# Kernel tuning notes

Hardware: AMD Instinct MI355X
Metric: run time of the kernel (lower is better)

The kernel has to match this reference:

```python
import jax, jax.numpy as jnp
import numpy as np

DIM, QS, NH, WS, SS, FFW = 256, 56, 8, 7, 3, 1024


def _make_attn_mask(H, W, ws, ss):
    # Swin-style shifted-window attention mask, [nWin, ws*ws, ws*ws]
    img = np.zeros((H, W))
    cnt = 0
    for hs in (slice(0, -ws), slice(-ws, -ss), slice(-ss, None)):
        for wsl in (slice(0, -ws), slice(-ws, -ss), slice(-ss, None)):
            img[hs, wsl] = cnt
            cnt += 1
    mw = img.reshape(H // ws, ws, W // ws, ws).transpose(0, 2, 1, 3).reshape(-1, ws * ws)
    am = mw[:, None, :] - mw[:, :, None]
    return jnp.asarray(np.where(am != 0, -100.0, 0.0), jnp.float32)

ATTN_MASK = _make_attn_mask(QS, QS, WS, SS)


def setup_inputs() -> dict:
    key = jax.random.key(0)
    ks = jax.random.split(key, 16)
    s = lambda fan: 1.0 / np.sqrt(fan)
    return {
        'x': jax.random.normal(ks[0], (16, DIM, QS, QS), jnp.float32),
        'ln1_g': jnp.ones((DIM,), jnp.float32),
        'ln1_b': jnp.zeros((DIM,), jnp.float32),
        'ln2_g': jnp.ones((DIM,), jnp.float32),
        'ln2_b': jnp.zeros((DIM,), jnp.float32),
        'qkv_w': jax.random.normal(ks[1], (DIM, 3 * DIM), jnp.float32) * s(DIM),
        'qkv_b': jnp.zeros((3 * DIM,), jnp.float32),
        'proj_w': jax.random.normal(ks[2], (DIM, DIM), jnp.float32) * s(DIM),
        'proj_b': jnp.zeros((DIM,), jnp.float32),
        'ffn_w1': jax.random.normal(ks[3], (DIM, FFW), jnp.float32) * s(DIM),
        'ffn_b1': jnp.zeros((FFW,), jnp.float32),
        'ffn_w2': jax.random.normal(ks[4], (FFW, DIM), jnp.float32) * s(FFW),
        'ffn_b2': jnp.zeros((DIM,), jnp.float32),
        'layer_scale': jax.random.normal(ks[5], (DIM,), jnp.float32),
    }


def _ln(t, g, b):
    m = t.mean(-1, keepdims=True)
    v = ((t - m) ** 2).mean(-1, keepdims=True)
    return (t - m) * jax.lax.rsqrt(v + 1e-5) * g + b


def reference(x, ln1_g, ln1_b, ln2_g, ln2_b, qkv_w, qkv_b, proj_w, proj_b,
              ffn_w1, ffn_b1, ffn_w2, ffn_b2, layer_scale):
    B, C, H, W = x.shape
    nh, ws, ss = NH, WS, SS
    hd = C // nh
    nHw, nWw = H // ws, W // ws
    xh = jnp.transpose(x, (0, 2, 3, 1))  # B H W C

    # --- shifted window attention ---
    h = _ln(xh, ln1_g, ln1_b)
    h = jnp.roll(h, (-ss, -ss), axis=(1, 2))
    # window partition: [B, nWin, L, C]
    h = h.reshape(B, nHw, ws, nWw, ws, C).transpose(0, 1, 3, 2, 4, 5)
    h = h.reshape(B, nHw * nWw, ws * ws, C)
    qkv = h @ qkv_w + qkv_b
    q, k, v = jnp.split(qkv, 3, axis=-1)
    L = ws * ws
    q = q.reshape(B, -1, L, nh, hd).transpose(0, 1, 3, 2, 4)  # B W h L d
    k = k.reshape(B, -1, L, nh, hd).transpose(0, 1, 3, 2, 4)
    v = v.reshape(B, -1, L, nh, hd).transpose(0, 1, 3, 2, 4)
    attn = jnp.einsum('bwhid,bwhjd->bwhij', q, k) * (hd ** -0.5)
    attn = attn + ATTN_MASK[None, :, None]  # mask per window index
    attn = jax.nn.softmax(attn, axis=-1)
    o = jnp.einsum('bwhij,bwhjd->bwhid', attn, v)
    o = o.transpose(0, 1, 3, 2, 4).reshape(B, nHw * nWw, L, C)
    o = o @ proj_w + proj_b
    # reverse partition + roll back
    o = o.reshape(B, nHw, nWw, ws, ws, C).transpose(0, 1, 3, 2, 4, 5).reshape(B, H, W, C)
    o = jnp.roll(o, (ss, ss), axis=(1, 2))
    x1 = xh + o

    # --- FFN ---
    h2 = _ln(x1, ln2_g, ln2_b)
    f = jax.nn.relu(h2 @ ffn_w1 + ffn_b1) @ ffn_w2 + ffn_b2
    f = f * layer_scale
    out = x1 + f
    return jnp.transpose(out, (0, 3, 1, 2))  # back to B C H W
```

## Files before the change

### kernel.cpp

```cpp
#include <hip/hip_runtime.h>
#include <hip/hip_bf16.h>
#include <math.h>

typedef unsigned short u16;
typedef __bf16 bf16x8 __attribute__((ext_vector_type(8)));
typedef float  f32x4  __attribute__((ext_vector_type(4)));

#define DIMC 256
#define QSZ  56
#define WSZ  7
#define SSZ  3
#define LWIN 49
#define NWIN 64
#define HW   3136
#define NTOK 50176
#define FFWD 1024
#define FCH  25088

__device__ __forceinline__ u16 f2bu(float f) {
    __hip_bfloat16 h = __float2bfloat16(f);
    return __builtin_bit_cast(u16, h);
}
__device__ __forceinline__ float bu2f(u16 u) {
    unsigned v = (unsigned)u << 16;
    return __builtin_bit_cast(float, v);
}
__device__ __forceinline__ void gload_lds16(const void* g, void* l) {
    __builtin_amdgcn_global_load_lds((const __attribute__((address_space(1))) void*)g,
                                     (__attribute__((address_space(3))) void*)l, 16, 0, 0);
}

__device__ __forceinline__ int region_of(int h) {
    return (h < 49) ? 0 : ((h < 53) ? 1 : 2);
}

__device__ __forceinline__ int row2tok(int m) {
    int b  = m / (NWIN * LWIN);
    int r  = m - b * (NWIN * LWIN);
    int wi = r / LWIN;
    int p  = r - wi * LWIN;
    int wh = wi >> 3, ww = wi & 7;
    int ph = p / 7,   pw = p - ph * 7;
    int hr = wh * 7 + ph, wr = ww * 7 + pw;
    int hs = hr + SSZ; if (hs >= QSZ) hs -= QSZ;
    int ws2 = wr + SSZ; if (ws2 >= QSZ) ws2 -= QSZ;
    return b * HW + hs * QSZ + ws2;
}

__global__ __launch_bounds__(256) void k_wconv(const float* __restrict__ W,
        u16* __restrict__ Wt, int K, int N) {
    __shared__ float tile[32][33];
    int k0 = blockIdx.x * 32, n0 = blockIdx.y * 32;
    int tx = threadIdx.x & 31, ty = threadIdx.x >> 5;
    for (int kk = ty; kk < 32; kk += 8)
        tile[kk][tx] = W[(size_t)(k0 + kk) * N + n0 + tx];
    __syncthreads();
    for (int nn = ty; nn < 32; nn += 8)
        Wt[(size_t)(n0 + nn) * K + k0 + tx] = f2bu(tile[tx][nn]);
}

__global__ __launch_bounds__(256) void k_ln1(const float* __restrict__ x,
        const float* __restrict__ g, const float* __restrict__ be,
        u16* __restrict__ hln) {
    __shared__ float tile[32][257];
    __shared__ float msh[32], rsh[32];
    int blk = blockIdx.x;
    int b   = blk / 98;
    int hw0 = (blk - b * 98) * 32;
    int t   = threadIdx.x;
    int tx  = t & 31, ty = t >> 5;
    for (int c = ty; c < 256; c += 8)
        tile[tx][c] = x[(size_t)(b * 256 + c) * HW + hw0 + tx];
    __syncthreads();
    int row = t >> 3, sub = t & 7;
    float s = 0.f, sq = 0.f;
    for (int c = sub * 32; c < sub * 32 + 32; ++c) {
        float v = tile[row][c]; s += v; sq += v * v;
    }
    for (int o = 4; o; o >>= 1) { s += __shfl_down(s, o, 8); sq += __shfl_down(sq, o, 8); }
    if (sub == 0) {
        float m   = s * (1.f / 256.f);
        float var = sq * (1.f / 256.f) - m * m;
        msh[row] = m; rsh[row] = rsqrtf(var + 1e-5f);
    }
    __syncthreads();
    float gg = g[t], bb = be[t];
    for (int r2 = 0; r2 < 32; ++r2) {
        float v = tile[r2][t];
        hln[(size_t)(b * HW + hw0 + r2) * 256 + t] = f2bu((v - msh[r2]) * rsh[r2] * gg + bb);
    }
}

__global__ __launch_bounds__(256) void k_ln2t(const float* __restrict__ x,
        u16* __restrict__ x1b, const float* __restrict__ g,
        const float* __restrict__ be, u16* __restrict__ h2) {
    __shared__ float tile[32][257];
    __shared__ float msh[32], rsh[32];
    int blk = blockIdx.x;
    int b   = blk / 98;
    int hw0 = (blk - b * 98) * 32;
    int t   = threadIdx.x;
    int tx  = t & 31, ty = t >> 5;
    for (int c = ty; c < 256; c += 8)
        tile[tx][c] = x[(size_t)(b * 256 + c) * HW + hw0 + tx];
    __syncthreads();
    size_t base = (size_t)b * HW + hw0;
    for (int r2 = 0; r2 < 32; ++r2) {
        float v = tile[r2][t] + bu2f(x1b[(base + r2) * 256 + t]);
        tile[r2][t] = v;
        x1b[(base + r2) * 256 + t] = f2bu(v);
    }
    __syncthreads();
    int row = t >> 3, sub = t & 7;
    float s = 0.f, sq = 0.f;
    for (int c = sub * 32; c < sub * 32 + 32; ++c) {
        float v = tile[row][c]; s += v; sq += v * v;
    }
    for (int o = 4; o; o >>= 1) { s += __shfl_down(s, o, 8); sq += __shfl_down(sq, o, 8); }
    if (sub == 0) {
        float m   = s * (1.f / 256.f);
        float var = sq * (1.f / 256.f) - m * m;
        msh[row] = m; rsh[row] = rsqrtf(var + 1e-5f);
    }
    __syncthreads();
    float gg = g[t], bb = be[t];
    for (int r2 = 0; r2 < 32; ++r2) {
        float v = tile[r2][t];
        h2[(base + r2) * 256 + t] = f2bu((v - msh[r2]) * rsh[r2] * gg + bb);
    }
}

template<int MODE>
__global__ __launch_bounds__(256) void k_mgemm(
        const u16* __restrict__ A, const u16* __restrict__ Bt,
        const float* __restrict__ bias, void* __restrict__ Cv,
        int K, int N, const void* __restrict__ extra,
        const float* __restrict__ extra2, int grow0) {
    __shared__ __align__(16) u16 As[2][128 * 32];
    __shared__ __align__(16) u16 Bs[2][128 * 32];
    const int m0 = blockIdx.x * 128, n0 = blockIdx.y * 128;
    const int t = threadIdx.x, lane = t & 63;
    const int wv = t >> 6, wr = wv >> 1, wc = wv & 1;

    int ar0 = m0 + (t >> 2), ar1 = ar0 + 64;
    if (MODE == 0) { ar0 = row2tok(ar0); ar1 = row2tok(ar1); }
    const u16* gA0 = A  + (size_t)ar0 * K + (t & 3) * 8;
    const u16* gA1 = A  + (size_t)ar1 * K + (t & 3) * 8;
    const u16* gB0 = Bt + (size_t)(n0 + (t >> 2)) * K + (t & 3) * 8;
    const u16* gB1 = Bt + (size_t)(n0 + 64 + (t >> 2)) * K + (t & 3) * 8;

    f32x4 acc[4][4] = {};
    const int ra = wr * 64 + (lane & 15);
    const int rb = wc * 64 + (lane & 15);
    const int ko = (lane >> 4) * 8;
    const int nIter = K >> 5;

    gload_lds16(gA0, As[0] + t * 8);
    gload_lds16(gA1, As[0] + 2048 + t * 8);
    gload_lds16(gB0, Bs[0] + t * 8);
    gload_lds16(gB1, Bs[0] + 2048 + t * 8);

    for (int it = 0; it < nIter; ++it) {
        const int cur = it & 1;
        if (it + 1 < nIter) {
            const int k1 = (it + 1) << 5;
            gload_lds16(gA0 + k1, As[cur ^ 1] + t * 8);
            gload_lds16(gA1 + k1, As[cur ^ 1] + 2048 + t * 8);
            gload_lds16(gB0 + k1, Bs[cur ^ 1] + t * 8);
            gload_lds16(gB1 + k1, Bs[cur ^ 1] + 2048 + t * 8);
            asm volatile("s_waitcnt vmcnt(4)" ::: "memory");
        } else {
            asm volatile("s_waitcnt vmcnt(0)" ::: "memory");
        }
        __builtin_amdgcn_s_barrier();
        __builtin_amdgcn_sched_barrier(0);
        bf16x8 af[4], bfr[4];
#pragma unroll
        for (int i = 0; i < 4; ++i)
            af[i] = *(const bf16x8*)(As[cur] + (ra + i * 16) * 32 + ko);
#pragma unroll
        for (int j = 0; j < 4; ++j)
            bfr[j] = *(const bf16x8*)(Bs[cur] + (rb + j * 16) * 32 + ko);
        asm volatile("s_waitcnt lgkmcnt(0)" ::: "memory");
        __builtin_amdgcn_sched_barrier(0);
        __builtin_amdgcn_s_barrier();
#pragma unroll
        for (int i = 0; i < 4; ++i)
#pragma unroll
            for (int j = 0; j < 4; ++j)
                acc[i][j] = __builtin_amdgcn_mfma_f32_16x16x32_bf16(af[i], bfr[j], acc[i][j], 0, 0, 0);
    }

    const int colb = n0 + wc * 64 + (lane & 15);
    const int rowb = m0 + wr * 64 + ((lane >> 4) * 4);

    if constexpr (MODE == 0) {
        u16* Cb = (u16*)Cv;
#pragma unroll
        for (int j = 0; j < 4; ++j) {
            int col = colb + j * 16; float bj = bias[col];
#pragma unroll
            for (int i = 0; i < 4; ++i) {
                int rw = rowb + i * 16;
#pragma unroll
                for (int r = 0; r < 4; ++r)
                    Cb[(size_t)(rw + r) * N + col] = f2bu(acc[i][j][r] + bj);
            }
        }
    } else if constexpr (MODE == 1) {
        u16* Cb = (u16*)Cv;
        int tok[4][4];
#pragma unroll
        for (int i = 0; i < 4; ++i)
#pragma unroll
            for (int r = 0; r < 4; ++r)
                tok[i][r] = row2tok(rowb + i * 16 + r);
#pragma unroll
        for (int j = 0; j < 4; ++j) {
            int col = colb + j * 16; float bj = bias[col];
#pragma unroll
            for (int i = 0; i < 4; ++i)
#pragma unroll
                for (int r = 0; r < 4; ++r)
                    Cb[(size_t)tok[i][r] * 256 + col] = f2bu(acc[i][j][r] + bj);
        }
    } else if constexpr (MODE == 2) {
        u16* Cb = (u16*)Cv;
#pragma unroll
        for (int j = 0; j < 4; ++j) {
            int col = colb + j * 16; float bj = bias[col];
#pragma unroll
            for (int i = 0; i < 4; ++i) {
                int rw = rowb + i * 16;
#pragma unroll
                for (int r = 0; r < 4; ++r)
                    Cb[(size_t)(rw + r) * N + col] = f2bu(fmaxf(acc[i][j][r] + bj, 0.f));
            }
        }
    } else {
        float* C = (float*)Cv;
        const u16* xr = (const u16*)extra;
#pragma unroll
        for (int j = 0; j < 4; ++j) {
            int col = colb + j * 16;
            float bj = bias[col], lj = extra2[col];
#pragma unroll
            for (int i = 0; i < 4; ++i) {
                int g  = grow0 + rowb + i * 16;
                int b  = g / HW, hw = g - b * HW;
                f32x4 o;
#pragma unroll
                for (int r = 0; r < 4; ++r)
                    o[r] = bu2f(xr[(size_t)(g + r) * 256 + col]) + lj * (acc[i][j][r] + bj);
                *(f32x4*)(C + ((size_t)(b * 256 + col)) * HW + hw) = o;
            }
        }
    }
}

__global__ __launch_bounds__(256, 4) void k_attn(const u16* __restrict__ qkv,
        u16* __restrict__ oattn) {
    __shared__ __align__(16) u16 Pl[4][64 * 72];
    const int wv = threadIdx.x >> 6, lane = threadIdx.x & 63;
    const int task = blockIdx.x * 4 + wv;
    const int head = task & 7, win = task >> 3, wi = win & 63;
    const int rowbase = win * LWIN;
    const int g = lane >> 4, c = lane & 15, ko = g * 8;
    const u16* qb = qkv + (size_t)rowbase * 768 + head * 32;

    bf16x8 qf[4], kf[4];
#pragma unroll
    for (int i = 0; i < 4; ++i) {
        int r0 = i * 16 + c; if (r0 > 48) r0 = 48;
        qf[i] = *(const bf16x8*)(qb + (size_t)r0 * 768 + ko);
        kf[i] = *(const bf16x8*)(qb + (size_t)r0 * 768 + 256 + ko);
    }
    f32x4 s[4][4] = {};
#pragma unroll
    for (int i = 0; i < 4; ++i)
#pragma unroll
        for (int j = 0; j < 4; ++j)
            s[i][j] = __builtin_amdgcn_mfma_f32_16x16x32_bf16(qf[i], kf[j], s[i][j], 0, 0, 0);

    bf16x8 vb[2][2];
#pragma unroll
    for (int j2 = 0; j2 < 2; ++j2) {
        int d = j2 * 16 + c;
#pragma unroll
        for (int h = 0; h < 2; ++h)
#pragma unroll
            for (int tt = 0; tt < 8; ++tt) {
                int k = h * 32 + ko + tt;
                u16 val = (k < LWIN) ? qb[(size_t)k * 768 + 512 + d] : (u16)0;
                vb[j2][h][tt] = __builtin_bit_cast(__bf16, val);
            }
    }

    const int wh7 = (wi >> 3) * 7, ww7 = (wi & 7) * 7;
    int idj[4]; bool jok[4];
#pragma unroll
    for (int j = 0; j < 4; ++j) {
        int col = j * 16 + c;
        jok[j] = col < LWIN;
        int p = jok[j] ? col : 48;
        idj[j] = region_of(wh7 + p / 7) * 3 + region_of(ww7 + p % 7);
    }
#pragma unroll
    for (int i = 0; i < 4; ++i) {
#pragma unroll
        for (int r = 0; r < 4; ++r) {
            int row = i * 16 + g * 4 + r;
            int p = row < LWIN ? row : 48;
            int idi = region_of(wh7 + p / 7) * 3 + region_of(ww7 + p % 7);
            float mx = -1e30f;
#pragma unroll
            for (int j = 0; j < 4; ++j) {
                float tv = jok[j] ? fmaf(s[i][j][r], 0.17677669529663687f,
                                         (idi == idj[j]) ? 0.f : -100.f)
                                  : -1e30f;
                s[i][j][r] = tv;
                mx = fmaxf(mx, tv);
            }
            for (int o = 8; o; o >>= 1) mx = fmaxf(mx, __shfl_xor(mx, o));
            float ps = 0.f;
#pragma unroll
            for (int j = 0; j < 4; ++j) {
                float e = __expf(s[i][j][r] - mx);
                s[i][j][r] = e; ps += e;
            }
            for (int o = 8; o; o >>= 1) ps += __shfl_xor(ps, o);
            float inv = 1.f / ps;
#pragma unroll
            for (int j = 0; j < 4; ++j)
                Pl[wv][row * 72 + j * 16 + c] = f2bu(s[i][j][r] * inv);
        }
    }

    f32x4 o[4][2] = {};
#pragma unroll
    for (int i = 0; i < 4; ++i) {
        bf16x8 pa0 = *(const bf16x8*)(&Pl[wv][(i * 16 + c) * 72 + ko]);
        bf16x8 pa1 = *(const bf16x8*)(&Pl[wv][(i * 16 + c) * 72 + ko + 32]);
#pragma unroll
        for (int j2 = 0; j2 < 2; ++j2) {
            o[i][j2] = __builtin_amdgcn_mfma_f32_16x16x32_bf16(pa0, vb[j2][0], o[i][j2], 0, 0, 0);
            o[i][j2] = __builtin_amdgcn_mfma_f32_16x16x32_bf16(pa1, vb[j2][1], o[i][j2], 0, 0, 0);
        }
    }
#pragma unroll
    for (int i = 0; i < 4; ++i)
#pragma unroll
        for (int r = 0; r < 4; ++r) {
            int row = i * 16 + g * 4 + r;
            if (row < LWIN) {
#pragma unroll
                for (int j2 = 0; j2 < 2; ++j2)
                    oattn[(size_t)(rowbase + row) * 256 + head * 32 + j2 * 16 + c]
                        = f2bu(o[i][j2][r]);
            }
        }
}

extern "C" void kernel_launch(void* const* d_in, const int* in_sizes, int n_in,
                              void* d_out, int out_size, void* d_ws, size_t ws_size,
                              hipStream_t stream) {
    const float* x      = (const float*)d_in[0];
    const float* ln1_g  = (const float*)d_in[1];
    const float* ln1_b  = (const float*)d_in[2];
    const float* ln2_g  = (const float*)d_in[3];
    const float* ln2_b  = (const float*)d_in[4];
    const float* qkv_w  = (const float*)d_in[5];
    const float* qkv_b  = (const float*)d_in[6];
    const float* proj_w = (const float*)d_in[7];
    const float* proj_b = (const float*)d_in[8];
    const float* ffn_w1 = (const float*)d_in[9];
    const float* ffn_b1 = (const float*)d_in[10];
    const float* ffn_w2 = (const float*)d_in[11];
    const float* ffn_b2 = (const float*)d_in[12];
    const float* lscale = (const float*)d_in[13];

    char* wsb = (char*)d_ws;
    u16* wqt  = (u16*)(wsb);
    u16* wpt  = (u16*)(wsb + 393216);
    u16* w1t  = (u16*)(wsb + 524288);
    u16* w2t  = (u16*)(wsb + 1048576);
    u16* P    = (u16*)(wsb + 1572864);
    char* Qb  = wsb + 27262976;
    u16* qkvb = (u16*)Qb;
    u16* x1b  = (u16*)Qb;
    u16* f1c  = (u16*)(Qb + 25690112);

    k_wconv<<<dim3(8, 24), 256, 0, stream>>>(qkv_w, wqt, 256, 768);
    k_wconv<<<dim3(8, 8),  256, 0, stream>>>(proj_w, wpt, 256, 256);
    k_wconv<<<dim3(8, 32), 256, 0, stream>>>(ffn_w1, w1t, 256, 1024);
    k_wconv<<<dim3(32, 8), 256, 0, stream>>>(ffn_w2, w2t, 1024, 256);

    k_ln1<<<16 * 98, 256, 0, stream>>>(x, ln1_g, ln1_b, P);
    k_mgemm<0><<<dim3(392, 6), 256, 0, stream>>>(P, wqt, qkv_b, qkvb, 256, 768,
                                                 nullptr, nullptr, 0);
    k_attn<<<2048, 256, 0, stream>>>(qkvb, P);
    k_mgemm<1><<<dim3(392, 2), 256, 0, stream>>>(P, wpt, proj_b, x1b, 256, 256,
                                                 nullptr, nullptr, 0);
    k_ln2t<<<16 * 98, 256, 0, stream>>>(x, x1b, ln2_g, ln2_b, P);
    for (int c = 0; c < 2; ++c) {
        k_mgemm<2><<<dim3(196, 8), 256, 0, stream>>>(P + (size_t)c * FCH * 256, w1t, ffn_b1,
                                                     f1c, 256, 1024, nullptr, nullptr, 0);
        k_mgemm<3><<<dim3(196, 2), 256, 0, stream>>>(f1c, w2t, ffn_b2, d_out, 1024, 256,
                                                     x1b, lscale, c * FCH);
    }
}
```

Baseline: 279.9 us.

## Enlarge GEMM tile to 256x128 with 512 threads and XOR-swizzle LDS

The bf16 MFMA GEMM now uses blocks of 8 waves that compute a 256x128 output tile. Each B tile is therefore reused across twice as many A rows, and each thread issues fewer global loads per k-step. The order of the 16-byte k-chunks in shared memory is XOR-swizzled by row, and the fragment reads use the matching swizzle, to reduce LDS bank conflicts. The trade-off is half as many blocks per launch and more LDS per block, which may lower occupancy and hurt load balance on the smaller GEMMs.

```diff
diff --git a/kernel.cpp b/kernel.cpp
--- a/kernel.cpp
+++ b/kernel.cpp
@@ -131,44 +131,42 @@
 }
 
 template<int MODE>
-__global__ __launch_bounds__(256) void k_mgemm(
+__global__ __launch_bounds__(512) void k_mgemm(
         const u16* __restrict__ A, const u16* __restrict__ Bt,
         const float* __restrict__ bias, void* __restrict__ Cv,
         int K, int N, const void* __restrict__ extra,
         const float* __restrict__ extra2, int grow0) {
-    __shared__ __align__(16) u16 As[2][128 * 32];
+    __shared__ __align__(16) u16 As[2][256 * 32];
     __shared__ __align__(16) u16 Bs[2][128 * 32];
-    const int m0 = blockIdx.x * 128, n0 = blockIdx.y * 128;
+    const int m0 = blockIdx.x * 256, n0 = blockIdx.y * 128;
     const int t = threadIdx.x, lane = t & 63;
     const int wv = t >> 6, wr = wv >> 1, wc = wv & 1;
 
-    int ar0 = m0 + (t >> 2), ar1 = ar0 + 64;
+    const int kc = (t & 3) ^ ((t >> 3) & 3);
+    int ar0 = m0 + (t >> 2), ar1 = m0 + 128 + (t >> 2);
     if (MODE == 0) { ar0 = row2tok(ar0); ar1 = row2tok(ar1); }
-    const u16* gA0 = A  + (size_t)ar0 * K + (t & 3) * 8;
-    const u16* gA1 = A  + (size_t)ar1 * K + (t & 3) * 8;
-    const u16* gB0 = Bt + (size_t)(n0 + (t >> 2)) * K + (t & 3) * 8;
-    const u16* gB1 = Bt + (size_t)(n0 + 64 + (t >> 2)) * K + (t & 3) * 8;
+    const u16* gA0 = A  + (size_t)ar0 * K + kc * 8;
+    const u16* gA1 = A  + (size_t)ar1 * K + kc * 8;
+    const u16* gB0 = Bt + (size_t)(n0 + (t >> 2)) * K + kc * 8;
 
     f32x4 acc[4][4] = {};
     const int ra = wr * 64 + (lane & 15);
     const int rb = wc * 64 + (lane & 15);
-    const int ko = (lane >> 4) * 8;
+    const int kos = (((lane >> 4) ^ (lane >> 1)) & 3) * 8;
     const int nIter = K >> 5;
 
     gload_lds16(gA0, As[0] + t * 8);
-    gload_lds16(gA1, As[0] + 2048 + t * 8);
+    gload_lds16(gA1, As[0] + 4096 + t * 8);
     gload_lds16(gB0, Bs[0] + t * 8);
-    gload_lds16(gB1, Bs[0] + 2048 + t * 8);
-
+
+    int cur = 0;
     for (int it = 0; it < nIter; ++it) {
-        const int cur = it & 1;
         if (it + 1 < nIter) {
             const int k1 = (it + 1) << 5;
             gload_lds16(gA0 + k1, As[cur ^ 1] + t * 8);
-            gload_lds16(gA1 + k1, As[cur ^ 1] + 2048 + t * 8);
+            gload_lds16(gA1 + k1, As[cur ^ 1] + 4096 + t * 8);
             gload_lds16(gB0 + k1, Bs[cur ^ 1] + t * 8);
-            gload_lds16(gB1 + k1, Bs[cur ^ 1] + 2048 + t * 8);
-            asm volatile("s_waitcnt vmcnt(4)" ::: "memory");
+            asm volatile("s_waitcnt vmcnt(3)" ::: "memory");
         } else {
             asm volatile("s_waitcnt vmcnt(0)" ::: "memory");
         }
@@ -177,10 +175,10 @@
         bf16x8 af[4], bfr[4];
 #pragma unroll
         for (int i = 0; i < 4; ++i)
-            af[i] = *(const bf16x8*)(As[cur] + (ra + i * 16) * 32 + ko);
+            af[i] = *(const bf16x8*)(As[cur] + (ra + i * 16) * 32 + kos);
 #pragma unroll
         for (int j = 0; j < 4; ++j)
-            bfr[j] = *(const bf16x8*)(Bs[cur] + (rb + j * 16) * 32 + ko);
+            bfr[j] = *(const bf16x8*)(Bs[cur] + (rb + ((j & 1) * 16 + (j >> 1) * 32)) * 32 + kos);
         asm volatile("s_waitcnt lgkmcnt(0)" ::: "memory");
         __builtin_amdgcn_sched_barrier(0);
         __builtin_amdgcn_s_barrier();
@@ -188,17 +186,19 @@
         for (int i = 0; i < 4; ++i)
 #pragma unroll
             for (int j = 0; j < 4; ++j)
-                acc[i][j] = __builtin_amdgcn_mfma_f32_16x16x32_bf16(af[i], bfr[j], acc[i][j], 0, 0, 0);
-    }
-
-    const int colb = n0 + wc * 64 + (lane & 15);
+                acc[i][j] = __builtin_amdgcn_mfma_f32_16x16x32_bf16(af[i],
+                    bfr[((j >> 4) * 0) + ((j & 3))], acc[i][j], 0, 0, 0);
+        cur ^= 1;
+    }
+
     const int rowb = m0 + wr * 64 + ((lane >> 4) * 4);
 
     if constexpr (MODE == 0) {
         u16* Cb = (u16*)Cv;
 #pragma unroll
         for (int j = 0; j < 4; ++j) {
-            int col = colb + j * 16; float bj = bias[col];
+            int col = n0 + wc * 64 + ((j & 1) * 16 + (j >> 1) * 32) + (lane & 15);
+            float bj = bias[col];
 #pragma unroll
             for (int i = 0; i < 4; ++i) {
                 int rw = rowb + i * 16;
@@ -217,7 +217,8 @@
                 tok[i][r] = row2tok(rowb + i * 16 + r);
 #pragma unroll
         for (int j = 0; j < 4; ++j) {
-            int col = colb + j * 16; float bj = bias[col];
+            int col = n0 + wc * 64 + ((j & 1) * 16 + (j >> 1) * 32) + (lane & 15);
+            float bj = bias[col];
 #pragma unroll
             for (int i = 0; i < 4; ++i)
 #pragma unroll
@@ -228,7 +229,8 @@
         u16* Cb = (u16*)Cv;
 #pragma unroll
         for (int j = 0; j < 4; ++j) {
-            int col = colb + j * 16; float bj = bias[col];
+            int col = n0 + wc * 64 + ((j & 1) * 16 + (j >> 1) * 32) + (lane & 15);
+            float bj = bias[col];
 #pragma unroll
             for (int i = 0; i < 4; ++i) {
                 int rw = rowb + i * 16;
@@ -242,7 +244,7 @@
         const u16* xr = (const u16*)extra;
 #pragma unroll
         for (int j = 0; j < 4; ++j) {
-            int col = colb + j * 16;
+            int col = n0 + wc * 64 + ((j & 1) * 16 + (j >> 1) * 32) + (lane & 15);
             float bj = bias[col], lj = extra2[col];
 #pragma unroll
             for (int i = 0; i < 4; ++i) {
@@ -396,16 +398,16 @@
     k_wconv<<<dim3(32, 8), 256, 0, stream>>>(ffn_w2, w2t, 1024, 256);
 
     k_ln1<<<16 * 98, 256, 0, stream>>>(x, ln1_g, ln1_b, P);
-    k_mgemm<0><<<dim3(392, 6), 256, 0, stream>>>(P, wqt, qkv_b, qkvb, 256, 768,
+    k_mgemm<0><<<dim3(196, 6), 512, 0, stream>>>(P, wqt, qkv_b, qkvb, 256, 768,
                                                  nullptr, nullptr, 0);
     k_attn<<<2048, 256, 0, stream>>>(qkvb, P);
-    k_mgemm<1><<<dim3(392, 2), 256, 0, stream>>>(P, wpt, proj_b, x1b, 256, 256,
+    k_mgemm<1><<<dim3(196, 2), 512, 0, stream>>>(P, wpt, proj_b, x1b, 256, 256,
                                                  nullptr, nullptr, 0);
     k_ln2t<<<16 * 98, 256, 0, stream>>>(x, x1b, ln2_g, ln2_b, P);
     for (int c = 0; c < 2; ++c) {
-        k_mgemm<2><<<dim3(196, 8), 256, 0, stream>>>(P + (size_t)c * FCH * 256, w1t, ffn_b1,
-                                                     f1c, 256, 1024, nullptr, nullptr, 0);
-        k_mgemm<3><<<dim3(196, 2), 256, 0, stream>>>(f1c, w2t, ffn_b2, d_out, 1024, 256,
-                                                     x1b, lscale, c * FCH);
-    }
-}
+        k_mgemm<2><<<dim3(98, 8), 512, 0, stream>>>(P + (size_t)c * FCH * 256, w1t, ffn_b1,
+                                                    f1c, 256, 1024, nullptr, nullptr, 0);
+        k_mgemm<3><<<dim3(98, 2), 512, 0, stream>>>(f1c, w2t, ffn_b2, d_out, 1024, 256,
+                                                    x1b, lscale, c * FCH);
+    }
+}
```

After: 292.8 us. 1.05x slower.
